# Performance work log

Measured on AMD Instinct MI355X. Metric: run time of the kernel, lower is better.

## Reference

```python
import jax, jax.numpy as jnp
import numpy as np
import math

B_ = 4
L_ = 2048
D_MODEL = 1024
D_STATE = 128
D_CONV = 4
HEADDIM = 64
CHUNK = 256
D_INNER = 2 * D_MODEL
NHEADS = D_INNER // HEADDIM
CONV_DIM = D_INNER + 2 * D_STATE
D_IN_PROJ = 2 * D_INNER + 2 * D_STATE + NHEADS


def setup_inputs() -> dict:
    key = jax.random.key(0)
    ks = jax.random.split(key, 8)
    u = jax.random.normal(ks[0], (B_, L_, D_MODEL), jnp.float32)
    W_in = jax.random.normal(ks[1], (D_IN_PROJ, D_MODEL), jnp.float32) * 0.02
    conv_w = jax.random.normal(ks[2], (CONV_DIM, D_CONV), jnp.float32) * 0.2
    conv_b = jnp.zeros((CONV_DIM,), jnp.float32)
    # dt init as in the torch module: dt ~ logU(0.001, 0.1), inverse-softplus
    dt = jnp.exp(jax.random.uniform(ks[3], (NHEADS,), jnp.float32) * (math.log(0.1) - math.log(0.001)) + math.log(0.001))
    dt = jnp.clip(dt, 1e-4, None)
    dt_bias = dt + jnp.log(-jnp.expm1(-dt))
    A_log = jnp.log(jax.random.uniform(ks[4], (NHEADS,), jnp.float32, minval=1.0, maxval=1.1))
    D_param = jnp.ones((NHEADS,), jnp.float32)
    norm_w = jnp.ones((D_INNER,), jnp.float32)
    W_out = jax.random.normal(ks[5], (D_MODEL, D_INNER), jnp.float32) * 0.02
    return {"u": u, "W_in": W_in, "conv_w": conv_w, "conv_b": conv_b,
            "dt_bias": dt_bias, "A_log": A_log, "D_param": D_param,
            "norm_w": norm_w, "W_out": W_out}


def _ssd(x, dt, A, Bm, Cm):
    """Chunked SSD scan (mamba_chunk_scan_combined math, ngroups=1).
    x: (b,l,h,p)  dt: (b,l,h) post-softplus  A: (h,)  Bm/Cm: (b,l,n)."""
    b, l, h, p = x.shape
    n = Bm.shape[-1]
    nc = l // CHUNK
    xr = x.reshape(b, nc, CHUNK, h, p)
    dtr = dt.reshape(b, nc, CHUNK, h)
    Br = Bm.reshape(b, nc, CHUNK, n)
    Cr = Cm.reshape(b, nc, CHUNK, n)
    dA = dtr * A                                    # (b,nc,cs,h), negative
    dA_cs = jnp.cumsum(dA, axis=2)                  # (b,nc,cs,h)
    # intra-chunk decay L[i,j] = exp(sum_{k=j+1..i} dA_k) for i >= j else 0
    diff = dA_cs[:, :, :, None, :] - dA_cs[:, :, None, :, :]  # (b,nc,i,j,h)
    mask = jnp.tril(jnp.ones((CHUNK, CHUNK), bool))
    Lmat = jnp.exp(jnp.where(mask[None, None, :, :, None], diff, -jnp.inf))
    dtx = dtr[..., None] * xr                       # (b,nc,cs,h,p)
    Y_diag = jnp.einsum('bcin,bcjn,bcijh,bcjhp->bcihp', Cr, Br, Lmat, dtx)
    # per-chunk final states
    decay_states = jnp.exp(dA_cs[:, :, -1:, :] - dA_cs)  # (b,nc,cs,h)
    states = jnp.einsum('bcjn,bcjh,bcjhp->bchpn', Br, decay_states, dtx)
    # inter-chunk recurrence over nc
    chunk_decay = jnp.exp(dA_cs[:, :, -1, :])       # (b,nc,h)
    def step(carry, inp):
        s, d = inp
        return carry * d[:, :, None, None] + s, carry
    init = jnp.zeros((b, h, p, n), x.dtype)
    _, prev = jax.lax.scan(step, init, (jnp.moveaxis(states, 1, 0), jnp.moveaxis(chunk_decay, 1, 0)))
    prev = jnp.moveaxis(prev, 0, 1)                 # (b,nc,h,p,n): state entering each chunk
    Y_off = jnp.einsum('bcin,bchpn,bcih->bcihp', Cr, prev, jnp.exp(dA_cs))
    return (Y_diag + Y_off).reshape(b, l, h, p)


def reference(u, W_in, conv_w, conv_b, dt_bias, A_log, D_param, norm_w, W_out):
    b, l, _ = u.shape
    zxbcdt = jnp.einsum('bld,ed->ble', u, W_in)     # (b,l,d_in_proj)
    z = zxbcdt[..., :D_INNER]
    xBC = zxbcdt[..., D_INNER:D_INNER + CONV_DIM]
    dt = zxbcdt[..., D_INNER + CONV_DIM:]
    # depthwise causal conv1d + SiLU
    xt = jnp.moveaxis(xBC, 1, 2)                    # (b,c,l)
    y = jax.lax.conv_general_dilated(xt, conv_w[:, None, :], (1,), [(D_CONV - 1, 0)], feature_group_count=CONV_DIM)
    xBC = jax.nn.silu(jnp.moveaxis(y + conv_b[None, :, None], 2, 1))
    x = xBC[..., :D_INNER].reshape(b, l, NHEADS, HEADDIM)
    Bm = xBC[..., D_INNER:D_INNER + D_STATE]
    Cm = xBC[..., D_INNER + D_STATE:]
    dt = jax.nn.softplus(dt + dt_bias)
    A = -jnp.exp(A_log)
    yh = _ssd(x, dt, A, Bm, Cm) + D_param[:, None] * x
    yf = yh.reshape(b, l, D_INNER)
    # gated RMSNorm (norm_before_gate=False): norm(y * silu(z)) * w
    g = yf * jax.nn.silu(z)
    g = g * jax.lax.rsqrt(jnp.mean(g * g, axis=-1, keepdims=True) + 1e-5) * norm_w
    return jnp.einsum('bld,ed->ble', g, W_out)
```

## Files before the change

kernel.cpp:

```cpp
#include <hip/hip_runtime.h>
#include <hip/hip_bf16.h>
#include <math.h>

#define B_N     4
#define L_N     2048
#define DMODEL  1024
#define DSTATE  128
#define DCONV   4
#define HEADDIM 64
#define CHUNK   256
#define DINNER  2048
#define NHEADS  32
#define CONVDIM 2304
#define DINPROJ 4384
#define NCHUNK  8
#define BL      (B_N*L_N)

typedef unsigned short ushort_t;
typedef unsigned int   uint_t;

typedef __attribute__((ext_vector_type(8))) short bf16x8;
typedef __attribute__((ext_vector_type(4))) float f32x4;

__device__ __forceinline__ float bfbits2f(ushort_t u){
    union { uint_t i; float f; } v; v.i = ((uint_t)u) << 16; return v.f;
}
__device__ __forceinline__ ushort_t f2bf(float f){
    union { float f; uint_t i; } v; v.f = f;
    uint_t r = v.i + 0x7FFF + ((v.i >> 16) & 1);
    return (ushort_t)(r >> 16);
}
__device__ __forceinline__ void gload_lds16(const void* g, void* l){
    __builtin_amdgcn_global_load_lds(
        (const __attribute__((address_space(1))) unsigned int*)g,
        (__attribute__((address_space(3))) unsigned int*)l, 16, 0, 0);
}

#define N_U8  (BL*DMODEL/8)
#define N_WI8 (DINPROJ*DMODEL/8)
#define N_WO8 (DMODEL*DINNER/8)

__global__ __launch_bounds__(256) void cvt_all(
    const float* __restrict__ u, const float* __restrict__ W_in,
    const float* __restrict__ W_out,
    ushort_t* __restrict__ u_bf, ushort_t* __restrict__ Wi_bf,
    ushort_t* __restrict__ Wo_bf)
{
    int i = blockIdx.x*256 + threadIdx.x;
    const float* src; ushort_t* dst; int off;
    if (i < N_U8)                { src = u;     dst = u_bf;  off = i; }
    else if (i < N_U8+N_WI8)     { src = W_in;  dst = Wi_bf; off = i - N_U8; }
    else if (i < N_U8+N_WI8+N_WO8){ src = W_out; dst = Wo_bf; off = i - N_U8 - N_WI8; }
    else return;
    const float4* p = (const float4*)(src + (size_t)off*8);
    float4 a = p[0], b = p[1];
    ushort_t o[8] = { f2bf(a.x), f2bf(a.y), f2bf(a.z), f2bf(a.w),
                      f2bf(b.x), f2bf(b.y), f2bf(b.z), f2bf(b.w) };
    *(uint4*)(dst + (size_t)off*8) = *(const uint4*)o;
}

__global__ __launch_bounds__(256) void cvt_wT(
    const float* __restrict__ cw, float* __restrict__ wT)
{
    int c = blockIdx.x*256 + threadIdx.x;
    if (c >= CONVDIM) return;
    float4 v = *(const float4*)&cw[c*DCONV];
    wT[0*CONVDIM + c] = v.x;
    wT[1*CONVDIM + c] = v.y;
    wT[2*CONVDIM + c] = v.z;
    wT[3*CONVDIM + c] = v.w;
}

template<int KDIM, int NTILES, int EPI>
__global__ __launch_bounds__(256) void gemm_bt_mfma(
    const ushort_t* __restrict__ A, const ushort_t* __restrict__ B,
    float* __restrict__ outf, ushort_t* __restrict__ z, ushort_t* __restrict__ xbc,
    const float* __restrict__ dt_bias, float* __restrict__ dtp)
{
    __shared__ __align__(16) ushort_t Asl[2][128*32];
    __shared__ __align__(16) ushort_t Bsl[2][128*32];

    int nwg = gridDim.x, cpx = nwg >> 3, lin = blockIdx.x;
    int work = (lin & 7)*cpx + (lin >> 3);
    int mtile = work / NTILES, ntile = work % NTILES;
    int m0 = mtile*128, n0 = ntile*128;

    int t = threadIdx.x;
    int l = t & 63, w = t >> 6;
    int wr = w >> 1, wc = w & 1;
    int lr16 = l & 15, kb = l >> 4;
    int srow = t >> 2, skc = (t & 3)*8;

    f32x4 acc[4][4];
    #pragma unroll
    for (int m=0;m<4;m++){
        #pragma unroll
        for (int n=0;n<4;n++) acc[m][n] = (f32x4){0.f,0.f,0.f,0.f};
    }

    int br0 = n0 + srow, br1 = n0 + 64 + srow;
    if (EPI == 1){
        br0 = (br0 < DINPROJ) ? br0 : (DINPROJ-1);
        br1 = (br1 < DINPROJ) ? br1 : (DINPROJ-1);
    }

    auto stage = [&](int buf, int k0){
        gload_lds16(A + (size_t)(m0+srow)*KDIM + k0 + skc,    &Asl[buf][t*8]);
        gload_lds16(A + (size_t)(m0+64+srow)*KDIM + k0 + skc, &Asl[buf][2048 + t*8]);
        gload_lds16(B + (size_t)br0*KDIM + k0 + skc,          &Bsl[buf][t*8]);
        gload_lds16(B + (size_t)br1*KDIM + k0 + skc,          &Bsl[buf][2048 + t*8]);
    };

    auto compute = [&](int cur){
        bf16x8 af[4], bfr[4];
        #pragma unroll
        for (int m=0;m<4;m++) af[m]  = *(const bf16x8*)&Asl[cur][(wr*64+m*16+lr16)*32 + kb*8];
        #pragma unroll
        for (int n=0;n<4;n++) bfr[n] = *(const bf16x8*)&Bsl[cur][(wc*64+n*16+lr16)*32 + kb*8];
        __builtin_amdgcn_s_setprio(1);
        #pragma unroll
        for (int m=0;m<4;m++){
            #pragma unroll
            for (int n=0;n<4;n++)
                acc[m][n] = __builtin_amdgcn_mfma_f32_16x16x32_bf16(af[m], bfr[n], acc[m][n], 0, 0, 0);
        }
        __builtin_amdgcn_s_setprio(0);
    };

    stage(0, 0);
    __syncthreads();
    int cur = 0;
    for (int k0=32; k0<KDIM; k0+=32){
        stage(cur^1, k0);
        compute(cur);
        __syncthreads();
        cur ^= 1;
    }
    compute(cur);

    #pragma unroll
    for (int m=0;m<4;m++){
        int rbase = m0 + wr*64 + m*16 + (l>>4)*4;
        #pragma unroll
        for (int n=0;n<4;n++){
            int gcol = n0 + wc*64 + n*16 + lr16;
            f32x4 v = acc[m][n];
            #pragma unroll
            for (int q=0;q<4;q++){
                int row = rbase + q;
                if (EPI == 0) {
                    outf[(size_t)row*DMODEL + gcol] = v[q];
                } else {
                    if (gcol < DINNER) {
                        z[(size_t)row*DINNER + gcol] = f2bf(v[q]);
                    } else if (gcol < DINNER + CONVDIM) {
                        xbc[(size_t)row*CONVDIM + (gcol - DINNER)] = f2bf(v[q]);
                    } else if (gcol < DINPROJ) {
                        int hh = gcol - (DINNER + CONVDIM);
                        float x = v[q] + dt_bias[hh];
                        float sp = (x > 15.f) ? x : log1pf(__expf(x));
                        int bb = row >> 11, ll = row & (L_N-1);
                        dtp[((size_t)bb*NHEADS + hh)*L_N + ll] = sp;
                    }
                }
            }
        }
    }
}

__global__ __launch_bounds__(256) void conv_silu(
    const __hip_bfloat16* __restrict__ xraw,
    const float* __restrict__ wT, const float* __restrict__ cb,
    __hip_bfloat16* __restrict__ xout)
{
    int idx = blockIdx.x*256 + threadIdx.x;
    int c8 = (idx % (CONVDIM/8))*8;
    int ml = idx / (CONVDIM/8);
    int b  = ml >> 11, l = ml & (L_N-1);
    const ushort_t* xr = (const ushort_t*)xraw;
    float acc[8];
    {
        float4 b0 = *(const float4*)&cb[c8];
        float4 b1 = *(const float4*)&cb[c8+4];
        acc[0]=b0.x; acc[1]=b0.y; acc[2]=b0.z; acc[3]=b0.w;
        acc[4]=b1.x; acc[5]=b1.y; acc[6]=b1.z; acc[7]=b1.w;
    }
    #pragma unroll
    for (int k=0;k<DCONV;k++){
        int li = l - (DCONV-1) + k;
        if (li >= 0){
            bf16x8 v = *(const bf16x8*)&xr[((size_t)b*L_N + li)*CONVDIM + c8];
            float4 w0 = *(const float4*)&wT[k*CONVDIM + c8];
            float4 w1 = *(const float4*)&wT[k*CONVDIM + c8 + 4];
            float wv[8] = {w0.x,w0.y,w0.z,w0.w,w1.x,w1.y,w1.z,w1.w};
            #pragma unroll
            for (int e=0;e<8;e++)
                acc[e] += wv[e] * bfbits2f(((const ushort_t*)&v)[e]);
        }
    }
    ushort_t o[8];
    #pragma unroll
    for (int e=0;e<8;e++){
        float s = acc[e] / (1.f + __expf(-acc[e]));
        o[e] = f2bf(s);
    }
    *(uint4*)((ushort_t*)xout + (size_t)idx*8) = *(const uint4*)o;
}

__global__ __launch_bounds__(256) void dt_cumsum(
    const float* __restrict__ dtp, const float* __restrict__ A_log,
    float* __restrict__ dAcs)
{
    int blk = blockIdx.x;
    int c  = blk % NCHUNK;
    int bh = blk / NCHUNK;
    int h  = bh & (NHEADS-1);
    int t  = threadIdx.x;
    float A = -__expf(A_log[h]);
    __shared__ float sm[CHUNK];
    float v = dtp[(size_t)bh*L_N + c*CHUNK + t] * A;
    sm[t] = v;
    __syncthreads();
    for (int off=1; off<CHUNK; off<<=1){
        float add = (t >= off) ? sm[t-off] : 0.f;
        __syncthreads();
        sm[t] += add;
        __syncthreads();
    }
    dAcs[(size_t)bh*L_N + c*CHUNK + t] = sm[t];
}

__global__ __launch_bounds__(256) void bc_scores_mfma(
    const __hip_bfloat16* __restrict__ xbc, ushort_t* __restrict__ S_T)
{
    __shared__ __align__(16) ushort_t Bs2[256*136];
    __shared__ __align__(16) ushort_t Cs2[256*136];
    int bc = blockIdx.x;
    int t = threadIdx.x;
    int l = t & 63, w = t >> 6;
    int l15 = l & 15, l4 = l >> 4;
    const ushort_t* xb = (const ushort_t*)xbc;
    const size_t rowbase = (size_t)bc*CHUNK*CONVDIM;

    #pragma unroll
    for (int ps=0; ps<16; ps++){
        int idx = ps*256 + t;
        int r = idx >> 4, ck = idx & 15;
        *(uint4*)&Bs2[r*136 + ck*8] =
            *(const uint4*)&xb[rowbase + (size_t)r*CONVDIM + DINNER + ck*8];
        *(uint4*)&Cs2[r*136 + ck*8] =
            *(const uint4*)&xb[rowbase + (size_t)r*CONVDIM + (DINNER+DSTATE) + ck*8];
    }
    __syncthreads();

    ushort_t* Sb = S_T + (size_t)bc*CHUNK*264;
    for (int if4 = w; if4 < 4; if4++){
        f32x4 acc[4][4];
        #pragma unroll
        for (int jf=0;jf<4;jf++){
            #pragma unroll
            for (int ir=0;ir<4;ir++) acc[jf][ir] = (f32x4){0.f,0.f,0.f,0.f};
        }
        #pragma unroll
        for (int k=0;k<4;k++){
            bf16x8 af[4], bfC[4];
            #pragma unroll
            for (int jf=0;jf<4;jf++)
                af[jf] = *(const bf16x8*)&Bs2[(w*64 + jf*16 + l15)*136 + k*32 + l4*8];
            #pragma unroll
            for (int ir=0;ir<4;ir++)
                bfC[ir] = *(const bf16x8*)&Cs2[(if4*64 + ir*16 + l15)*136 + k*32 + l4*8];
            #pragma unroll
            for (int jf=0;jf<4;jf++){
                #pragma unroll
                for (int ir=0;ir<4;ir++)
                    acc[jf][ir] = __builtin_amdgcn_mfma_f32_16x16x32_bf16(af[jf], bfC[ir], acc[jf][ir], 0, 0, 0);
            }
        }
        #pragma unroll
        for (int jf=0;jf<4;jf++){
            #pragma unroll
            for (int ir=0;ir<4;ir++){
                #pragma unroll
                for (int q=0;q<4;q++){
                    int j = w*64 + jf*16 + l4*4 + q;
                    int i = if4*64 + ir*16 + l15;
                    Sb[(size_t)j*264 + i] = f2bf(acc[jf][ir][q]);
                }
            }
        }
    }
}

__device__ __forceinline__ int swz264(int row, int col){
    return row*264 + (col ^ (((row>>3)&7)<<3));
}

__global__ __launch_bounds__(256) void ssd_states_mfma(
    const __hip_bfloat16* __restrict__ xbc,
    const float* __restrict__ dtp, const float* __restrict__ dAcs,
    float* __restrict__ states)
{
    __shared__ __align__(16) ushort_t xdT[64*264];
    __shared__ __align__(16) ushort_t BT[128*264];
    __shared__ float coef_s[CHUNK];
    int bc = blockIdx.x, hg = blockIdx.y;
    int b = bc >> 3, c = bc & 7;
    int t = threadIdx.x;
    int l = t & 63, w = t >> 6;
    int l15 = l & 15, l4 = l >> 4;
    const ushort_t* xb = (const ushort_t*)xbc;
    const size_t rowbase = (size_t)bc*CHUNK*CONVDIM;

    #pragma unroll
    for (int ps=0; ps<16; ps++){
        int idx = ps*256 + t;
        int j = idx >> 4, n0 = (idx & 15)*8;
        bf16x8 v = *(const bf16x8*)&xb[rowbase + (size_t)j*CONVDIM + DINNER + n0];
        #pragma unroll
        for (int e=0;e<8;e++)
            BT[swz264(n0+e, j)] = ((const ushort_t*)&v)[e];
    }

    for (int hh=0; hh<4; hh++){
        int h = hg*4 + hh;
        size_t dbase = ((size_t)b*NHEADS + h)*L_N + c*CHUNK;
        float last = dAcs[dbase + CHUNK-1];
        float cf = __expf(last - dAcs[dbase + t]) * dtp[dbase + t];
        coef_s[t] = cf;
        __syncthreads();

        #pragma unroll
        for (int ps=0; ps<8; ps++){
            int idx = ps*256 + t;
            int j = idx >> 3, p0 = (idx & 7)*8;
            float cj = coef_s[j];
            bf16x8 v = *(const bf16x8*)&xb[rowbase + (size_t)j*CONVDIM + h*HEADDIM + p0];
            #pragma unroll
            for (int e=0;e<8;e++)
                xdT[swz264(p0+e, j)] = f2bf(cj * bfbits2f(((const ushort_t*)&v)[e]));
        }
        __syncthreads();

        f32x4 acc[4][2];
        #pragma unroll
        for (int pf=0;pf<4;pf++){
            #pragma unroll
            for (int nf=0;nf<2;nf++) acc[pf][nf] = (f32x4){0.f,0.f,0.f,0.f};
        }

        #pragma unroll
        for (int k=0;k<8;k++){
            bf16x8 af[4], bv[2];
            #pragma unroll
            for (int pf=0;pf<4;pf++)
                af[pf] = *(const bf16x8*)&xdT[swz264(pf*16 + l15, k*32 + l4*8)];
            #pragma unroll
            for (int nf=0;nf<2;nf++)
                bv[nf] = *(const bf16x8*)&BT[swz264(w*32 + nf*16 + l15, k*32 + l4*8)];
            #pragma unroll
            for (int pf=0;pf<4;pf++){
                #pragma unroll
                for (int nf=0;nf<2;nf++)
                    acc[pf][nf] = __builtin_amdgcn_mfma_f32_16x16x32_bf16(af[pf], bv[nf], acc[pf][nf], 0, 0, 0);
            }
        }

        float* sb = states + (size_t)(bc*NHEADS + h)*HEADDIM*DSTATE;
        #pragma unroll
        for (int pf=0;pf<4;pf++){
            #pragma unroll
            for (int nf=0;nf<2;nf++){
                #pragma unroll
                for (int q=0;q<4;q++){
                    int p = pf*16 + l4*4 + q;
                    int n = w*32 + nf*16 + l15;
                    sb[(size_t)p*DSTATE + n] = acc[pf][nf][q];
                }
            }
        }
    }
}

__global__ __launch_bounds__(256) void scan_states(
    float* __restrict__ states, const float* __restrict__ dAcs)
{
    int idx = blockIdx.x*256 + threadIdx.x;
    int n  = idx & 127;
    int p  = (idx >> 7) & 63;
    int bh = idx >> 13;
    int b  = bh >> 5, h = bh & 31;
    float carry = 0.f;
    for (int c=0;c<NCHUNK;c++){
        size_t off = (((size_t)((b*NCHUNK + c)*NHEADS + h))*HEADDIM + p)*DSTATE + n;
        float s = states[off];
        states[off] = carry;
        float cd = __expf(dAcs[((size_t)b*NHEADS + h)*L_N + c*CHUNK + (CHUNK-1)]);
        carry = carry * cd + s;
    }
}

__global__ __launch_bounds__(256) void ssd_mfma(
    const __hip_bfloat16* __restrict__ xbc,
    const float* __restrict__ dtp, const float* __restrict__ dAcs,
    const float* __restrict__ states, const ushort_t* __restrict__ S_T,
    const float* __restrict__ D_param, ushort_t* __restrict__ yh)
{
    __shared__ __align__(16) ushort_t Ws[256*72];
    __shared__ __align__(16) ushort_t xdT[64*264];
    __shared__ float da_s[CHUNK];
    __shared__ float dt_s[CHUNK];

    int bc = blockIdx.x, h = blockIdx.y;
    int b = bc >> 3, c = bc & 7;
    int t = threadIdx.x;
    int l = t & 63, w = t >> 6;
    int l15 = l & 15, l4 = l >> 4;

    const ushort_t* xb = (const ushort_t*)xbc;
    const size_t rowbase = (size_t)bc*CHUNK*CONVDIM;

    da_s[t] = dAcs[((size_t)b*NHEADS + h)*L_N + c*CHUNK + t];
    dt_s[t] = dtp[((size_t)b*NHEADS + h)*L_N + c*CHUNK + t];

    #pragma unroll
    for (int ps=0; ps<8; ps++){
        int idx = ps*256 + t;
        int j = idx >> 3, p0 = (idx & 7)*8;
        bf16x8 v = *(const bf16x8*)&xb[rowbase + (size_t)j*CONVDIM + h*HEADDIM + p0];
        #pragma unroll
        for (int e=0;e<8;e++) xdT[(p0+e)*264 + j] = ((const ushort_t*)&v)[e];
    }
    __syncthreads();

    f32x4 yacc[4][4];
    #pragma unroll
    for (int m=0;m<4;m++){
        #pragma unroll
        for (int np=0;np<4;np++) yacc[m][np] = (f32x4){0.f,0.f,0.f,0.f};
    }

    const ushort_t* cbase = xb + rowbase + (size_t)l15*CONVDIM + (DINNER+DSTATE) + l4*8;
    const float*    pbase = states + (size_t)(bc*NHEADS + h)*HEADDIM*DSTATE
                                   + (size_t)l15*DSTATE + l4*8;
    #pragma unroll
    for (int k=0;k<4;k++){
        bf16x8 bfk[4];
        #pragma unroll
        for (int np=0;np<4;np++){
            const float* pr = pbase + (size_t)(np*16)*DSTATE + k*32;
            float4 a = *(const float4*)pr;
            float4 bq = *(const float4*)(pr + 4);
            bf16x8 r;
            r[0]=(short)f2bf(a.x);  r[1]=(short)f2bf(a.y);
            r[2]=(short)f2bf(a.z);  r[3]=(short)f2bf(a.w);
            r[4]=(short)f2bf(bq.x); r[5]=(short)f2bf(bq.y);
            r[6]=(short)f2bf(bq.z); r[7]=(short)f2bf(bq.w);
            bfk[np] = r;
        }
        #pragma unroll
        for (int m=0;m<4;m++){
            int i0 = (m*4 + w)*16;
            bf16x8 af = *(const bf16x8*)(cbase + (size_t)i0*CONVDIM + k*32);
            #pragma unroll
            for (int np=0;np<4;np++)
                yacc[m][np] = __builtin_amdgcn_mfma_f32_16x16x32_bf16(af, bfk[np], yacc[m][np], 0, 0, 0);
        }
    }
    #pragma unroll
    for (int m=0;m<4;m++){
        int i0 = (m*4 + w)*16;
        #pragma unroll
        for (int q=0;q<4;q++){
            float e = __expf(da_s[i0 + l4*4 + q]);
            #pragma unroll
            for (int np=0;np<4;np++) yacc[m][np][q] *= e;
        }
    }

    const ushort_t* Sb = S_T + (size_t)bc*CHUNK*264;
    for (int jp=0; jp<4; jp++){
        bf16x8 bfx[4][2];
        #pragma unroll
        for (int np=0;np<4;np++){
            #pragma unroll
            for (int ks=0;ks<2;ks++)
                bfx[np][ks] = *(const bf16x8*)&xdT[(np*16 + l15)*264 + jp*64 + ks*32 + l4*8];
        }

        #pragma unroll
        for (int m=0;m<4;m++){
            int i0 = (m*4 + w)*16;
            int imax = i0 + 15;
            int kmaxY = (jp*64 <= imax ? 1 : 0) + (jp*64+32 <= imax ? 1 : 0);
            if (kmaxY == 0) continue;
            int nmax = 2*kmaxY;

            float dai[4];
            #pragma unroll
            for (int q=0;q<4;q++) dai[q] = da_s[i0 + l4*4 + q];
            #pragma unroll
            for (int n=0;n<4;n++){
                if (n < nmax){
                    int jcol = jp*64 + n*16 + l15;
                    float daj = da_s[jcol], dtj = dt_s[jcol];
                    ushort_t sv[4];
                    *(uint2*)sv = *(const uint2*)&Sb[(size_t)jcol*264 + i0 + l4*4];
                    #pragma unroll
                    for (int q=0;q<4;q++){
                        int i = i0 + l4*4 + q;
                        float wv = 0.f;
                        if (jcol <= i) wv = __expf(dai[q] - daj) * dtj * bfbits2f(sv[q]);
                        Ws[i*72 + n*16 + l15] = f2bf(wv);
                    }
                }
            }
            #pragma unroll
            for (int ks=0;ks<2;ks++){
                if (ks < kmaxY){
                    bf16x8 wfA = *(const bf16x8*)&Ws[(i0 + l15)*72 + ks*32 + l4*8];
                    #pragma unroll
                    for (int np=0;np<4;np++)
                        yacc[m][np] = __builtin_amdgcn_mfma_f32_16x16x32_bf16(wfA, bfx[np][ks], yacc[m][np], 0, 0, 0);
                }
            }
        }
    }

    float Dh = D_param[h];
    #pragma unroll
    for (int m=0;m<4;m++){
        int i0 = (m*4 + w)*16;
        #pragma unroll
        for (int np=0;np<4;np++){
            int p = np*16 + l15;
            #pragma unroll
            for (int q=0;q<4;q++){
                int i = i0 + l4*4 + q;
                float xv = bfbits2f(xdT[p*264 + i]);
                yh[((size_t)bc*CHUNK + i)*DINNER + h*HEADDIM + p] = f2bf(yacc[m][np][q] + Dh*xv);
            }
        }
    }
}

__global__ __launch_bounds__(256) void gate_norm(
    const ushort_t* __restrict__ yh, const __hip_bfloat16* __restrict__ z,
    const float* __restrict__ norm_w, __hip_bfloat16* __restrict__ g)
{
    int row = blockIdx.x;
    int t = threadIdx.x;
    const ushort_t* yr = yh + (size_t)row*DINNER + t*8;
    const ushort_t* zr = (const ushort_t*)z + (size_t)row*DINNER + t*8;
    bf16x8 yv = *(const bf16x8*)yr;
    bf16x8 zv8 = *(const bf16x8*)zr;
    float v[8];
    float ss = 0.f;
    #pragma unroll
    for (int e=0;e<8;e++){
        float y = bfbits2f(((const ushort_t*)&yv)[e]);
        float zz = bfbits2f(((const ushort_t*)&zv8)[e]);
        float gv = y * (zz / (1.f + __expf(-zz)));
        v[e] = gv; ss += gv*gv;
    }
    #pragma unroll
    for (int off=32; off>=1; off>>=1) ss += __shfl_xor(ss, off);
    __shared__ float red[4];
    if ((t & 63) == 0) red[t >> 6] = ss;
    __syncthreads();
    float tot = red[0]+red[1]+red[2]+red[3];
    float scale = rsqrtf(tot * (1.f/DINNER) + 1e-5f);
    float4 w0 = *(const float4*)&norm_w[t*8];
    float4 w1 = *(const float4*)&norm_w[t*8+4];
    float nw[8] = {w0.x,w0.y,w0.z,w0.w,w1.x,w1.y,w1.z,w1.w};
    ushort_t o[8];
    #pragma unroll
    for (int e=0;e<8;e++) o[e] = f2bf(v[e]*scale*nw[e]);
    *(uint4*)((ushort_t*)g + (size_t)row*DINNER + t*8) = *(const uint4*)o;
}

extern "C" void kernel_launch(void* const* d_in, const int* in_sizes, int n_in,
                              void* d_out, int out_size, void* d_ws, size_t ws_size,
                              hipStream_t stream)
{
    const float* u       = (const float*)d_in[0];
    const float* W_in    = (const float*)d_in[1];
    const float* conv_w  = (const float*)d_in[2];
    const float* conv_b  = (const float*)d_in[3];
    const float* dt_bias = (const float*)d_in[4];
    const float* A_log   = (const float*)d_in[5];
    const float* D_param = (const float*)d_in[6];
    const float* norm_w  = (const float*)d_in[7];
    const float* W_out   = (const float*)d_in[8];
    float* out = (float*)d_out;

    char* p = (char*)d_ws;
    auto take = [&](size_t n){ char* r = p; p += (n + 255) & ~(size_t)255; return r; };

    __hip_bfloat16* z       = (__hip_bfloat16*)take((size_t)BL*DINNER*2);
    __hip_bfloat16* xbc_raw = (__hip_bfloat16*)take((size_t)BL*CONVDIM*2);
    __hip_bfloat16* xbc     = (__hip_bfloat16*)take((size_t)BL*CONVDIM*2);
    float* dtp     = (float*)take((size_t)BL*NHEADS*4);
    float* dAcs    = (float*)take((size_t)BL*NHEADS*4);
    float* states  = (float*)take((size_t)B_N*NCHUNK*NHEADS*HEADDIM*DSTATE*4);
    ushort_t* yh   = (ushort_t*)take((size_t)BL*DINNER*2);
    ushort_t* S_T  = (ushort_t*)take((size_t)B_N*NCHUNK*CHUNK*264*2);
    ushort_t* u_bf  = (ushort_t*)take((size_t)BL*DMODEL*2);
    ushort_t* Wi_bf = (ushort_t*)take((size_t)DINPROJ*DMODEL*2);
    ushort_t* Wo_bf = (ushort_t*)take((size_t)DMODEL*DINNER*2);
    float* wT       = (float*)take((size_t)DCONV*CONVDIM*4);
    __hip_bfloat16* g = z;

    cvt_all<<<dim3((N_U8+N_WI8+N_WO8 + 255)/256), 256, 0, stream>>>(
        u, W_in, W_out, u_bf, Wi_bf, Wo_bf);
    cvt_wT<<<dim3((CONVDIM+255)/256), 256, 0, stream>>>(conv_w, wT);

    gemm_bt_mfma<DMODEL,35,1><<<dim3(64*35), 256, 0, stream>>>(
        u_bf, Wi_bf, nullptr, (ushort_t*)z, (ushort_t*)xbc_raw, dt_bias, dtp);

    conv_silu<<<dim3(BL*(CONVDIM/8)/256), 256, 0, stream>>>(xbc_raw, wT, conv_b, xbc);
    dt_cumsum<<<dim3(B_N*NHEADS*NCHUNK), 256, 0, stream>>>(dtp, A_log, dAcs);
    bc_scores_mfma<<<dim3(B_N*NCHUNK), 256, 0, stream>>>(xbc, S_T);
    ssd_states_mfma<<<dim3(B_N*NCHUNK, NHEADS/4), 256, 0, stream>>>(xbc, dtp, dAcs, states);
    scan_states<<<dim3((B_N*NHEADS*HEADDIM*DSTATE)/256), 256, 0, stream>>>(states, dAcs);
    ssd_mfma<<<dim3(B_N*NCHUNK, NHEADS), 256, 0, stream>>>(xbc, dtp, dAcs, states, S_T, D_param, yh);
    gate_norm<<<dim3(BL), 256, 0, stream>>>(yh, z, norm_w, g);

    gemm_bt_mfma<DINNER,8,0><<<dim3(64*8), 256, 0, stream>>>(
        (const ushort_t*)g, Wo_bf, out, nullptr, nullptr, nullptr, nullptr);
}
```

Measured before the change: 368.0 us.

## Compute two conv outputs per thread, store scanned states as bf16, add MFMA priority hints

The conv+SiLU kernel now has each thread produce two consecutive timesteps. It reuses the five loaded input rows and hoists the weight loads, which halves redundant global reads. The scan kernel writes its carried states directly as bf16 into a new buffer, so ssd_mfma loads bf16 fragments directly without the fp32 load and convert. s_setprio hints are also placed around the MFMA blocks in the state and output kernels, and the A-fragment loads are hoisted. Together these cut memory traffic and instruction overhead in several small kernels. The cost is extra workspace, plus scheduling hints that may do nothing.

```diff
diff --git a/kernel.cpp b/kernel.cpp
--- a/kernel.cpp
+++ b/kernel.cpp
@@ -176,35 +176,55 @@
     int idx = blockIdx.x*256 + threadIdx.x;
     int c8 = (idx % (CONVDIM/8))*8;
     int ml = idx / (CONVDIM/8);
-    int b  = ml >> 11, l = ml & (L_N-1);
+    int b  = ml / (L_N/2);
+    int l  = (ml % (L_N/2))*2;
     const ushort_t* xr = (const ushort_t*)xraw;
-    float acc[8];
+
+    float wv[4][8];
+    #pragma unroll
+    for (int k=0;k<DCONV;k++){
+        float4 w0 = *(const float4*)&wT[k*CONVDIM + c8];
+        float4 w1 = *(const float4*)&wT[k*CONVDIM + c8 + 4];
+        wv[k][0]=w0.x; wv[k][1]=w0.y; wv[k][2]=w0.z; wv[k][3]=w0.w;
+        wv[k][4]=w1.x; wv[k][5]=w1.y; wv[k][6]=w1.z; wv[k][7]=w1.w;
+    }
+    float bias[8];
     {
         float4 b0 = *(const float4*)&cb[c8];
         float4 b1 = *(const float4*)&cb[c8+4];
-        acc[0]=b0.x; acc[1]=b0.y; acc[2]=b0.z; acc[3]=b0.w;
-        acc[4]=b1.x; acc[5]=b1.y; acc[6]=b1.z; acc[7]=b1.w;
-    }
-    #pragma unroll
-    for (int k=0;k<DCONV;k++){
-        int li = l - (DCONV-1) + k;
+        bias[0]=b0.x; bias[1]=b0.y; bias[2]=b0.z; bias[3]=b0.w;
+        bias[4]=b1.x; bias[5]=b1.y; bias[6]=b1.z; bias[7]=b1.w;
+    }
+
+    float xv[5][8];
+    #pragma unroll
+    for (int r=0;r<5;r++){
+        int li = l - 3 + r;
         if (li >= 0){
             bf16x8 v = *(const bf16x8*)&xr[((size_t)b*L_N + li)*CONVDIM + c8];
-            float4 w0 = *(const float4*)&wT[k*CONVDIM + c8];
-            float4 w1 = *(const float4*)&wT[k*CONVDIM + c8 + 4];
-            float wv[8] = {w0.x,w0.y,w0.z,w0.w,w1.x,w1.y,w1.z,w1.w};
-            #pragma unroll
-            for (int e=0;e<8;e++)
-                acc[e] += wv[e] * bfbits2f(((const ushort_t*)&v)[e]);
-        }
-    }
-    ushort_t o[8];
+            #pragma unroll
+            for (int e=0;e<8;e++) xv[r][e] = bfbits2f(((const ushort_t*)&v)[e]);
+        } else {
+            #pragma unroll
+            for (int e=0;e<8;e++) xv[r][e] = 0.f;
+        }
+    }
+
+    ushort_t o0[8], o1[8];
     #pragma unroll
     for (int e=0;e<8;e++){
-        float s = acc[e] / (1.f + __expf(-acc[e]));
-        o[e] = f2bf(s);
-    }
-    *(uint4*)((ushort_t*)xout + (size_t)idx*8) = *(const uint4*)o;
+        float a0 = bias[e], a1 = bias[e];
+        #pragma unroll
+        for (int k=0;k<DCONV;k++){
+            a0 += wv[k][e]*xv[k][e];
+            a1 += wv[k][e]*xv[k+1][e];
+        }
+        o0[e] = f2bf(a0 / (1.f + __expf(-a0)));
+        o1[e] = f2bf(a1 / (1.f + __expf(-a1)));
+    }
+    ushort_t* ob = (ushort_t*)xout + ((size_t)b*L_N + l)*CONVDIM + c8;
+    *(uint4*)ob = *(const uint4*)o0;
+    *(uint4*)(ob + CONVDIM) = *(const uint4*)o1;
 }
 
 __global__ __launch_bounds__(256) void dt_cumsum(
@@ -358,12 +378,14 @@
             #pragma unroll
             for (int nf=0;nf<2;nf++)
                 bv[nf] = *(const bf16x8*)&BT[swz264(w*32 + nf*16 + l15, k*32 + l4*8)];
+            __builtin_amdgcn_s_setprio(1);
             #pragma unroll
             for (int pf=0;pf<4;pf++){
                 #pragma unroll
                 for (int nf=0;nf<2;nf++)
                     acc[pf][nf] = __builtin_amdgcn_mfma_f32_16x16x32_bf16(af[pf], bv[nf], acc[pf][nf], 0, 0, 0);
             }
+            __builtin_amdgcn_s_setprio(0);
         }
 
         float* sb = states + (size_t)(bc*NHEADS + h)*HEADDIM*DSTATE;
@@ -383,7 +405,8 @@
 }
 
 __global__ __launch_bounds__(256) void scan_states(
-    float* __restrict__ states, const float* __restrict__ dAcs)
+    const float* __restrict__ states, const float* __restrict__ dAcs,
+    ushort_t* __restrict__ prev_bf)
 {
     int idx = blockIdx.x*256 + threadIdx.x;
     int n  = idx & 127;
@@ -393,8 +416,8 @@
     float carry = 0.f;
     for (int c=0;c<NCHUNK;c++){
         size_t off = (((size_t)((b*NCHUNK + c)*NHEADS + h))*HEADDIM + p)*DSTATE + n;
+        prev_bf[off] = f2bf(carry);
         float s = states[off];
-        states[off] = carry;
         float cd = __expf(dAcs[((size_t)b*NHEADS + h)*L_N + c*CHUNK + (CHUNK-1)]);
         carry = carry * cd + s;
     }
@@ -403,7 +426,7 @@
 __global__ __launch_bounds__(256) void ssd_mfma(
     const __hip_bfloat16* __restrict__ xbc,
     const float* __restrict__ dtp, const float* __restrict__ dAcs,
-    const float* __restrict__ states, const ushort_t* __restrict__ S_T,
+    const ushort_t* __restrict__ prev_bf, const ushort_t* __restrict__ S_T,
     const float* __restrict__ D_param, ushort_t* __restrict__ yh)
 {
     __shared__ __align__(16) ushort_t Ws[256*72];
@@ -441,31 +464,27 @@
     }
 
     const ushort_t* cbase = xb + rowbase + (size_t)l15*CONVDIM + (DINNER+DSTATE) + l4*8;
-    const float*    pbase = states + (size_t)(bc*NHEADS + h)*HEADDIM*DSTATE
-                                   + (size_t)l15*DSTATE + l4*8;
+    const ushort_t* pbase = prev_bf + (size_t)(bc*NHEADS + h)*HEADDIM*DSTATE
+                                    + (size_t)l15*DSTATE + l4*8;
     #pragma unroll
     for (int k=0;k<4;k++){
         bf16x8 bfk[4];
         #pragma unroll
+        for (int np=0;np<4;np++)
+            bfk[np] = *(const bf16x8*)(pbase + (size_t)(np*16)*DSTATE + k*32);
+        bf16x8 af0 = *(const bf16x8*)(cbase + (size_t)((0*4+w)*16)*CONVDIM + k*32);
+        bf16x8 af1 = *(const bf16x8*)(cbase + (size_t)((1*4+w)*16)*CONVDIM + k*32);
+        bf16x8 af2 = *(const bf16x8*)(cbase + (size_t)((2*4+w)*16)*CONVDIM + k*32);
+        bf16x8 af3 = *(const bf16x8*)(cbase + (size_t)((3*4+w)*16)*CONVDIM + k*32);
+        __builtin_amdgcn_s_setprio(1);
+        #pragma unroll
         for (int np=0;np<4;np++){
-            const float* pr = pbase + (size_t)(np*16)*DSTATE + k*32;
-            float4 a = *(const float4*)pr;
-            float4 bq = *(const float4*)(pr + 4);
-            bf16x8 r;
-            r[0]=(short)f2bf(a.x);  r[1]=(short)f2bf(a.y);
-            r[2]=(short)f2bf(a.z);  r[3]=(short)f2bf(a.w);
-            r[4]=(short)f2bf(bq.x); r[5]=(short)f2bf(bq.y);
-            r[6]=(short)f2bf(bq.z); r[7]=(short)f2bf(bq.w);
-            bfk[np] = r;
-        }
-        #pragma unroll
-        for (int m=0;m<4;m++){
-            int i0 = (m*4 + w)*16;
-            bf16x8 af = *(const bf16x8*)(cbase + (size_t)i0*CONVDIM + k*32);
-            #pragma unroll
-            for (int np=0;np<4;np++)
-                yacc[m][np] = __builtin_amdgcn_mfma_f32_16x16x32_bf16(af, bfk[np], yacc[m][np], 0, 0, 0);
-        }
+            yacc[0][np] = __builtin_amdgcn_mfma_f32_16x16x32_bf16(af0, bfk[np], yacc[0][np], 0, 0, 0);
+            yacc[1][np] = __builtin_amdgcn_mfma_f32_16x16x32_bf16(af1, bfk[np], yacc[1][np], 0, 0, 0);
+            yacc[2][np] = __builtin_amdgcn_mfma_f32_16x16x32_bf16(af2, bfk[np], yacc[2][np], 0, 0, 0);
+            yacc[3][np] = __builtin_amdgcn_mfma_f32_16x16x32_bf16(af3, bfk[np], yacc[3][np], 0, 0, 0);
+        }
+        __builtin_amdgcn_s_setprio(0);
     }
     #pragma unroll
     for (int m=0;m<4;m++){
@@ -515,6 +534,7 @@
                     }
                 }
             }
+            __builtin_amdgcn_s_setprio(1);
             #pragma unroll
             for (int ks=0;ks<2;ks++){
                 if (ks < kmaxY){
@@ -524,6 +544,7 @@
                         yacc[m][np] = __builtin_amdgcn_mfma_f32_16x16x32_bf16(wfA, bfx[np][ks], yacc[m][np], 0, 0, 0);
                 }
             }
+            __builtin_amdgcn_s_setprio(0);
         }
     }
 
@@ -603,6 +624,7 @@
     float* dtp     = (float*)take((size_t)BL*NHEADS*4);
     float* dAcs    = (float*)take((size_t)BL*NHEADS*4);
     float* states  = (float*)take((size_t)B_N*NCHUNK*NHEADS*HEADDIM*DSTATE*4);
+    ushort_t* prev_bf = (ushort_t*)take((size_t)B_N*NCHUNK*NHEADS*HEADDIM*DSTATE*2);
     ushort_t* yh   = (ushort_t*)take((size_t)BL*DINNER*2);
     ushort_t* S_T  = (ushort_t*)take((size_t)B_N*NCHUNK*CHUNK*264*2);
     ushort_t* u_bf  = (ushort_t*)take((size_t)BL*DMODEL*2);
@@ -618,12 +640,12 @@
     gemm_bt_mfma<DMODEL,35,1><<<dim3(64*35), 256, 0, stream>>>(
         u_bf, Wi_bf, nullptr, (ushort_t*)z, (ushort_t*)xbc_raw, dt_bias, dtp);
 
-    conv_silu<<<dim3(BL*(CONVDIM/8)/256), 256, 0, stream>>>(xbc_raw, wT, conv_b, xbc);
+    conv_silu<<<dim3((BL/2)*(CONVDIM/8)/256), 256, 0, stream>>>(xbc_raw, wT, conv_b, xbc);
     dt_cumsum<<<dim3(B_N*NHEADS*NCHUNK), 256, 0, stream>>>(dtp, A_log, dAcs);
     bc_scores_mfma<<<dim3(B_N*NCHUNK), 256, 0, stream>>>(xbc, S_T);
     ssd_states_mfma<<<dim3(B_N*NCHUNK, NHEADS/4), 256, 0, stream>>>(xbc, dtp, dAcs, states);
-    scan_states<<<dim3((B_N*NHEADS*HEADDIM*DSTATE)/256), 256, 0, stream>>>(states, dAcs);
-    ssd_mfma<<<dim3(B_N*NCHUNK, NHEADS), 256, 0, stream>>>(xbc, dtp, dAcs, states, S_T, D_param, yh);
+    scan_states<<<dim3((B_N*NHEADS*HEADDIM*DSTATE)/256), 256, 0, stream>>>(states, dAcs, prev_bf);
+    ssd_mfma<<<dim3(B_N*NCHUNK, NHEADS), 256, 0, stream>>>(xbc, dtp, dAcs, prev_bf, S_T, D_param, yh);
     gate_norm<<<dim3(BL), 256, 0, stream>>>(yh, z, norm_w, g);
 
     gemm_bt_mfma<DINNER,8,0><<<dim3(64*8), 256, 0, stream>>>(
```

Result: faster. 352.5 us (-4.2%).
